# Kernel tuning notes

Hardware: AMD Instinct MI355X
Metric: run time of the kernel (lower is better)

The kernel has to match this reference:

```python
import jax, jax.numpy as jnp
import numpy as np

V = 100000  # num graph nodes
E = 800000  # num edges (avg degree 8)
B = 16      # batch
C = 16      # in == hidden == out channels (forced by residual adds)
K = 4       # Chebyshev order
EPS = 1e-5


def setup_inputs() -> dict:
    key = jax.random.key(0)
    ks = jax.random.split(key, 8)
    x = jax.random.normal(ks[0], (B, C, V), jnp.float32)
    edge_src = jax.random.randint(ks[1], (E,), 0, V, dtype=jnp.int32)
    edge_dst = jax.random.randint(ks[2], (E,), 0, V, dtype=jnp.int32)
    # small positive weights keep the Chebyshev recursion numerically tame
    edge_w = jax.random.uniform(ks[3], (E,), jnp.float32) * 0.1
    weights = jax.random.normal(ks[4], (6, K, C, C), jnp.float32) * (1.0 / np.sqrt(K * C))
    biases = jax.random.normal(ks[5], (6, C), jnp.float32) * 0.01
    gamma = jnp.ones((5, C), jnp.float32)
    beta = jnp.zeros((5, C), jnp.float32)
    return {"x": x, "edge_w": edge_w, "weights": weights, "biases": biases,
            "gamma": gamma, "beta": beta, "edge_src": edge_src, "edge_dst": edge_dst}


def reference(x, edge_w, weights, biases, gamma, beta, edge_src, edge_dst):
    def lap(xf):  # normalized laplacian apply: (2/lmax)*L - I with lmax=2 -> L - I; xf: (V, F)
        msg = xf[edge_src] * edge_w[:, None]
        return jax.ops.segment_sum(msg, edge_dst, num_segments=V) - xf

    def cheb(xin, w, b):  # xin: (B, Cin, V), w: (K, Cin, Cout), b: (Cout,)
        Cin = xin.shape[1]
        xf = xin.transpose(2, 0, 1).reshape(V, B * Cin)  # (V, B*Cin)
        x0 = xf
        xs = [x0]
        x1 = lap(x0)
        xs.append(x1)
        for _ in range(K - 2):
            x2 = 2.0 * lap(x1) - x0
            xs.append(x2)
            x0, x1 = x1, x2
        xk = jnp.stack(xs).reshape(K, V, B, Cin)
        out = jnp.einsum('kvbi,kio->bov', xk, w) + b[None, :, None]
        return out  # (B, Cout, V)

    def bn(xin, g, bt):  # BatchNorm1d over (B, C, V): stats over (B, V)
        mean = xin.mean(axis=(0, 2), keepdims=True)
        var = xin.var(axis=(0, 2), keepdims=True)
        return (xin - mean) * jax.lax.rsqrt(var + EPS) * g[None, :, None] + bt[None, :, None]

    def resblock(xin, i, bni):
        h = jax.nn.relu(cheb(xin, weights[2 * i], biases[2 * i]))
        h = bn(h, gamma[bni], beta[bni])
        h = cheb(h, weights[2 * i + 1], biases[2 * i + 1])
        return jax.nn.relu(h + xin)

    out = resblock(x, 0, 0)
    out = bn(out, gamma[3], beta[3])
    out = resblock(out, 1, 1)
    out = bn(out, gamma[4], beta[4])
    out = resblock(out, 2, 2)
    pooled = out.max(axis=2)  # MaxPool1d(num_nodes) + squeeze -> (B, C)
    return jax.nn.softmax(pooled, axis=1)
```

## Files before the change

kernel.cpp:

```cpp
#include <hip/hip_runtime.h>
#include <hip/hip_fp16.h>
#include <cstdint>

#define CAP 32
#define WAVES 4

typedef __half half_t;

__device__ __forceinline__ float4 ldh4(const half_t* p) {
  uint2 u = *reinterpret_cast<const uint2*>(p);
  __half2 h0 = *reinterpret_cast<const __half2*>(&u.x);
  __half2 h1 = *reinterpret_cast<const __half2*>(&u.y);
  float2 f0 = __half22float2(h0);
  float2 f1 = __half22float2(h1);
  return make_float4(f0.x, f0.y, f1.x, f1.y);
}

__device__ __forceinline__ void sth4(half_t* p, float x, float y, float z, float w) {
  __half2 h0 = __floats2half2_rn(x, y);
  __half2 h1 = __floats2half2_rn(z, w);
  uint2 u;
  u.x = *reinterpret_cast<unsigned int*>(&h0);
  u.y = *reinterpret_cast<unsigned int*>(&h1);
  *reinterpret_cast<uint2*>(p) = u;
}

__global__ __launch_bounds__(256) void transpose_kernel(
    const float* __restrict__ in, half_t* __restrict__ out, int V) {
  __shared__ float t[32][33];
  const int f0 = blockIdx.y * 32;
  const int v0 = blockIdx.x * 32;
  const int tid = threadIdx.x;
  const int fi = tid >> 5;
  const int vi = tid & 31;
#pragma unroll
  for (int k = 0; k < 4; ++k) {
    int f = fi + 8 * k;
    t[f][vi] = in[(size_t)(f0 + f) * V + (v0 + vi)];
  }
  __syncthreads();
  const int vl = tid >> 5;
  const int fl = tid & 31;
#pragma unroll
  for (int k = 0; k < 4; ++k) {
    int v = vl + 8 * k;
    out[(size_t)(v0 + v) * 256 + (f0 + fl)] = __float2half_rn(t[fl][v]);
  }
}

__global__ __launch_bounds__(256) void fill_kernel(
    const int* __restrict__ src, const int* __restrict__ dst,
    const float* __restrict__ w, int* __restrict__ cursor,
    int2* __restrict__ slots, int E) {
  int e = blockIdx.x * 256 + threadIdx.x;
  if (e >= E) return;
  int d = dst[e];
  int pos = atomicAdd(&cursor[d], 1);
  if (pos < CAP) slots[(size_t)d * CAP + pos] = make_int2(src[e], __float_as_int(w[e]));
}

template <int PASS, int EPI>
__global__ __launch_bounds__(256) void cheb_pass(
    const half_t* __restrict__ G, const half_t* __restrict__ Pv,
    half_t* __restrict__ D, half_t* __restrict__ O,
    const half_t* __restrict__ resid,
    const int2* __restrict__ slots, const int* __restrict__ cnt,
    const float* __restrict__ Wl, const float* __restrict__ bl,
    float* __restrict__ statsBuf, int V) {
  __shared__ float xl[WAVES][272];
  __shared__ float wl[512];
  const int tid = threadIdx.x;
  if (PASS == 1) {
    wl[tid] = Wl[tid];
    wl[256 + tid] = Wl[256 + tid];
  } else if (PASS == 2) {
    wl[tid] = Wl[512 + tid];
  } else {
    wl[tid] = Wl[768 + tid];
  }
  __syncthreads();
  const int wave = tid >> 6, lane = tid & 63;
  const int v = blockIdx.x * WAVES + wave;
  if (v >= V) return;
  const int f0 = lane << 2;
  int n = cnt[v];
  n = n > CAP ? CAP : n;
  const int2* __restrict__ row = slots + (size_t)v * CAP;
  float4 acc = make_float4(0.f, 0.f, 0.f, 0.f);
  int e = 0;
  for (; e + 2 <= n; e += 2) {
    int2 s0 = row[e];
    int2 s1 = row[e + 1];
    float w0 = __int_as_float(s0.y), w1 = __int_as_float(s1.y);
    float4 a = ldh4(G + (((size_t)s0.x) << 8) + f0);
    float4 b2 = ldh4(G + (((size_t)s1.x) << 8) + f0);
    acc.x = fmaf(w0, a.x, acc.x); acc.y = fmaf(w0, a.y, acc.y);
    acc.z = fmaf(w0, a.z, acc.z); acc.w = fmaf(w0, a.w, acc.w);
    acc.x = fmaf(w1, b2.x, acc.x); acc.y = fmaf(w1, b2.y, acc.y);
    acc.z = fmaf(w1, b2.z, acc.z); acc.w = fmaf(w1, b2.w, acc.w);
  }
  if (e < n) {
    int2 s0 = row[e];
    float w0 = __int_as_float(s0.y);
    float4 a = ldh4(G + (((size_t)s0.x) << 8) + f0);
    acc.x = fmaf(w0, a.x, acc.x); acc.y = fmaf(w0, a.y, acc.y);
    acc.z = fmaf(w0, a.z, acc.z); acc.w = fmaf(w0, a.w, acc.w);
  }
  const size_t rowoff = (((size_t)v) << 8) + f0;
  float4 g = ldh4(G + rowoff);
  float4 xn;
  if (PASS == 1) {
    xn.x = acc.x - g.x; xn.y = acc.y - g.y; xn.z = acc.z - g.z; xn.w = acc.w - g.w;
  } else {
    float4 p = ldh4(Pv + rowoff);
    xn.x = 2.f * (acc.x - g.x) - p.x;
    xn.y = 2.f * (acc.y - g.y) - p.y;
    xn.z = 2.f * (acc.z - g.z) - p.z;
    xn.w = 2.f * (acc.w - g.w) - p.w;
  }
  if (PASS != 3) {
    sth4(D + rowoff, xn.x, xn.y, xn.z, xn.w);
  }
  const int b = lane >> 2;
  const int oc = (lane & 3) << 2;
  float* xw = xl[wave];
  const int sbase = f0 + b;
  float o[4];
  if (PASS == 1) {
    o[0] = bl[oc + 0]; o[1] = bl[oc + 1]; o[2] = bl[oc + 2]; o[3] = bl[oc + 3];
    xw[sbase + 0] = g.x; xw[sbase + 1] = g.y; xw[sbase + 2] = g.z; xw[sbase + 3] = g.w;
    __builtin_amdgcn_wave_barrier();
    const float* xb = xw + b * 17;
#pragma unroll
    for (int i = 0; i < 16; ++i) {
      float xi = xb[i];
      o[0] = fmaf(xi, wl[i * 16 + oc + 0], o[0]);
      o[1] = fmaf(xi, wl[i * 16 + oc + 1], o[1]);
      o[2] = fmaf(xi, wl[i * 16 + oc + 2], o[2]);
      o[3] = fmaf(xi, wl[i * 16 + oc + 3], o[3]);
    }
    __builtin_amdgcn_wave_barrier();
  } else {
    o[0] = o[1] = o[2] = o[3] = 0.f;
  }
  xw[sbase + 0] = xn.x; xw[sbase + 1] = xn.y; xw[sbase + 2] = xn.z; xw[sbase + 3] = xn.w;
  __builtin_amdgcn_wave_barrier();
  {
    const float* xb = xw + b * 17;
    const float* wm = (PASS == 1) ? (wl + 256) : wl;
#pragma unroll
    for (int i = 0; i < 16; ++i) {
      float xi = xb[i];
      o[0] = fmaf(xi, wm[i * 16 + oc + 0], o[0]);
      o[1] = fmaf(xi, wm[i * 16 + oc + 1], o[1]);
      o[2] = fmaf(xi, wm[i * 16 + oc + 2], o[2]);
      o[3] = fmaf(xi, wm[i * 16 + oc + 3], o[3]);
    }
  }
  half_t* op = O + rowoff;
  if (PASS == 1) {
    sth4(op, o[0], o[1], o[2], o[3]);
  } else if (PASS == 2) {
    float4 c4 = ldh4(op);
    sth4(op, o[0] + c4.x, o[1] + c4.y, o[2] + c4.z, o[3] + c4.w);
  } else {
    float4 c4 = ldh4(op);
    o[0] += c4.x; o[1] += c4.y; o[2] += c4.z; o[3] += c4.w;
    if (EPI >= 2) {
      float4 r = ldh4(resid + rowoff);
      o[0] += r.x; o[1] += r.y; o[2] += r.z; o[3] += r.w;
    }
    o[0] = fmaxf(o[0], 0.f); o[1] = fmaxf(o[1], 0.f);
    o[2] = fmaxf(o[2], 0.f); o[3] = fmaxf(o[3], 0.f);
    sth4(op, o[0], o[1], o[2], o[3]);
    if (EPI == 1 || EPI == 2) {
      float s0 = o[0], s1 = o[1], s2 = o[2], s3 = o[3];
      float q0 = o[0] * o[0], q1 = o[1] * o[1], q2 = o[2] * o[2], q3 = o[3] * o[3];
#pragma unroll
      for (int d = 4; d < 64; d <<= 1) {
        s0 += __shfl_xor(s0, d); s1 += __shfl_xor(s1, d);
        s2 += __shfl_xor(s2, d); s3 += __shfl_xor(s3, d);
        q0 += __shfl_xor(q0, d); q1 += __shfl_xor(q1, d);
        q2 += __shfl_xor(q2, d); q3 += __shfl_xor(q3, d);
      }
      if (lane < 4) {
        float* sb = statsBuf + ((blockIdx.x & 63) << 5);
        atomicAdd(&sb[(lane << 2) + 0], s0);
        atomicAdd(&sb[(lane << 2) + 1], s1);
        atomicAdd(&sb[(lane << 2) + 2], s2);
        atomicAdd(&sb[(lane << 2) + 3], s3);
        atomicAdd(&sb[16 + (lane << 2) + 0], q0);
        atomicAdd(&sb[16 + (lane << 2) + 1], q1);
        atomicAdd(&sb[16 + (lane << 2) + 2], q2);
        atomicAdd(&sb[16 + (lane << 2) + 3], q3);
      }
    }
  }
}

__global__ void bn_finalize(const float* __restrict__ sb,
                            const float* __restrict__ gamma,
                            const float* __restrict__ beta,
                            float* __restrict__ affine, float invN) {
  int c = threadIdx.x;
  if (c >= 16) return;
  float s = 0.f, q = 0.f;
  for (int k = 0; k < 64; ++k) { s += sb[k * 32 + c]; q += sb[k * 32 + 16 + c]; }
  float mean = s * invN;
  float var = q * invN - mean * mean;
  float inv = rsqrtf(var + 1e-5f);
  float A = gamma[c] * inv;
  float B = beta[c] - mean * A;
  affine[c] = A;
  affine[16 + c] = B;
}

__global__ __launch_bounds__(256) void bn_apply(half_t* __restrict__ X,
                                                const float* __restrict__ affine,
                                                size_t NT) {
  size_t i0 = ((size_t)blockIdx.x * 256 + threadIdx.x) * 8;
  size_t stride = (size_t)gridDim.x * 256 * 8;
  float a[8], bb[8];
#pragma unroll
  for (int j = 0; j < 8; ++j) {
    int c = (int)((i0 + j) & 15);
    a[j] = affine[c];
    bb[j] = affine[16 + c];
  }
  for (size_t i = i0; i < NT; i += stride) {
    uint4 u = *reinterpret_cast<uint4*>(X + i);
    __half2* h = reinterpret_cast<__half2*>(&u);
#pragma unroll
    for (int j = 0; j < 4; ++j) {
      float2 f = __half22float2(h[j]);
      f.x = fmaf(a[2 * j], f.x, bb[2 * j]);
      f.y = fmaf(a[2 * j + 1], f.y, bb[2 * j + 1]);
      h[j] = __floats2half2_rn(f.x, f.y);
    }
    *reinterpret_cast<uint4*>(X + i) = u;
  }
}

__global__ __launch_bounds__(256) void pool_kernel(const half_t* __restrict__ X,
                                                   float* __restrict__ part, int V) {
  int t = threadIdx.x;
  float m = -3.402823466e38f;
  for (int v = blockIdx.x; v < V; v += gridDim.x) {
    m = fmaxf(m, __half2float(X[(((size_t)v) << 8) + t]));
  }
  part[blockIdx.x * 256 + t] = m;
}

__global__ __launch_bounds__(256) void pool_finish(const float* __restrict__ part,
                                                   float* __restrict__ out) {
  int t = threadIdx.x;
  float m = -3.402823466e38f;
  for (int k = 0; k < 256; ++k) m = fmaxf(m, part[k * 256 + t]);
  __shared__ float pm[256];
  __shared__ float mx[16], sm[16];
  pm[t] = m;
  __syncthreads();
  if (t < 16) {
    float M = -3.402823466e38f;
    for (int c = 0; c < 16; ++c) M = fmaxf(M, pm[t * 16 + c]);
    float S = 0.f;
    for (int c = 0; c < 16; ++c) S += expf(pm[t * 16 + c] - M);
    mx[t] = M;
    sm[t] = S;
  }
  __syncthreads();
  out[t] = expf(pm[t] - mx[t >> 4]) / sm[t >> 4];
}

__global__ void sentinel_kernel(float* out, float val) {
  out[threadIdx.x] = val;
}

extern "C" void kernel_launch(void* const* d_in, const int* in_sizes, int n_in,
                              void* d_out, int out_size, void* d_ws, size_t ws_size,
                              hipStream_t stream) {
  const float* x       = (const float*)d_in[0];
  const float* edge_w  = (const float*)d_in[1];
  const float* weights = (const float*)d_in[2];
  const float* biases  = (const float*)d_in[3];
  const float* gamma   = (const float*)d_in[4];
  const float* beta    = (const float*)d_in[5];
  const int*   esrc    = (const int*)d_in[6];
  const int*   edst    = (const int*)d_in[7];

  const int V = in_sizes[0] / 256;
  const int E = in_sizes[1];
  const size_t NT = (size_t)V * 256;

  char* wsp = (char*)d_ws;
  auto carve = [&](size_t bytes) {
    char* p = wsp;
    wsp += (bytes + 255) & ~(size_t)255;
    return p;
  };
  half_t* P[4];
  for (int i = 0; i < 4; ++i) P[i] = (half_t*)carve(NT * sizeof(half_t));
  int2*  slots  = (int2*)carve((size_t)V * CAP * sizeof(int2));
  int*   cursor = (int*)carve((size_t)V * sizeof(int));
  float* stats  = (float*)carve(5 * 64 * 32 * sizeof(float));
  float* affine = (float*)carve(5 * 32 * sizeof(float));
  float* part   = (float*)carve(256 * 256 * sizeof(float));
  size_t needed = (size_t)(wsp - (char*)d_ws);
  if (needed > ws_size) {
    sentinel_kernel<<<1, 256, 0, stream>>>((float*)d_out, 100.0f + (float)(needed >> 20));
    return;
  }

  hipMemsetAsync(cursor, 0, (size_t)V * sizeof(int), stream);
  hipMemsetAsync(stats, 0, 5 * 64 * 32 * sizeof(float), stream);

  dim3 tg(V / 32, 8, 1);
  transpose_kernel<<<tg, 256, 0, stream>>>(x, P[0], V);
  fill_kernel<<<(E + 255) / 256, 256, 0, stream>>>(esrc, edst, edge_w, cursor, slots, E);

  const int nb = (V + WAVES - 1) / WAVES;
  const float invN = 1.f / (16.f * (float)V);

  half_t *C = P[0], *X = P[1], *Y = P[2], *Z = P[3];
  for (int blk = 0; blk < 3; ++blk) {
    const float* WA = weights + (size_t)(2 * blk) * 1024;
    const float* WB = weights + (size_t)(2 * blk + 1) * 1024;
    const float* bA = biases + (2 * blk) * 16;
    const float* bB = biases + (2 * blk + 1) * 16;
    float* stA = stats + blk * 2048;
    float* afA = affine + blk * 32;
    cheb_pass<1, 0><<<nb, 256, 0, stream>>>(C, nullptr, X, Y, nullptr, slots, cursor, WA, bA, nullptr, V);
    cheb_pass<2, 0><<<nb, 256, 0, stream>>>(X, C, Z, Y, nullptr, slots, cursor, WA, nullptr, nullptr, V);
    cheb_pass<3, 1><<<nb, 256, 0, stream>>>(Z, X, nullptr, Y, nullptr, slots, cursor, WA, nullptr, stA, V);
    bn_finalize<<<1, 16, 0, stream>>>(stA, gamma + blk * 16, beta + blk * 16, afA, invN);
    bn_apply<<<2048, 256, 0, stream>>>(Y, afA, NT);
    cheb_pass<1, 0><<<nb, 256, 0, stream>>>(Y, nullptr, X, Z, nullptr, slots, cursor, WB, bB, nullptr, V);
    cheb_pass<2, 0><<<nb, 256, 0, stream>>>(X, Y, Y, Z, nullptr, slots, cursor, WB, nullptr, nullptr, V);
    if (blk < 2) {
      float* stI = stats + (3 + blk) * 2048;
      float* afI = affine + (3 + blk) * 32;
      cheb_pass<3, 2><<<nb, 256, 0, stream>>>(Y, X, nullptr, Z, C, slots, cursor, WB, nullptr, stI, V);
      bn_finalize<<<1, 16, 0, stream>>>(stI, gamma + (3 + blk) * 16, beta + (3 + blk) * 16, afI, invN);
      bn_apply<<<2048, 256, 0, stream>>>(Z, afI, NT);
    } else {
      cheb_pass<3, 3><<<nb, 256, 0, stream>>>(Y, X, nullptr, Z, C, slots, cursor, WB, nullptr, nullptr, V);
    }
    half_t* oC = C; half_t* oY = Y; half_t* oZ = Z;
    C = oZ; Y = oC; Z = oY;
  }
  pool_kernel<<<256, 256, 0, stream>>>(C, part, V);
  pool_finish<<<1, 256, 0, stream>>>(part, (float*)d_out);
}
```

Before: 2.374 ms.

## Batch edge slot loads via wave shuffles and unroll gathers by eight

Each wave now loads its node's 32 slot entries once, one per lane, and broadcasts source index and weight with shuffles. The neighbor loop is padded to a multiple of 8, with dummy slots pre-initialised to a self-index and zero weight, so eight independent gathers can be in flight at once. The self and previous-term loads are hoisted to the top of the kernel. This trades a new init kernel that writes all V*CAP slots, plus wasted padded gathers, for more memory-level parallelism in the sparse gather.

```diff
diff --git a/kernel.cpp b/kernel.cpp
--- a/kernel.cpp
+++ b/kernel.cpp
@@ -46,6 +46,11 @@
     int v = vl + 8 * k;
     out[(size_t)(v0 + v) * 256 + (f0 + fl)] = __float2half_rn(t[fl][v]);
   }
+}
+
+__global__ __launch_bounds__(256) void init_slots(int2* __restrict__ slots, int total) {
+  int i = blockIdx.x * 256 + threadIdx.x;
+  if (i < total) slots[i] = make_int2(i >> 5, 0);
 }
 
 __global__ __launch_bounds__(256) void fill_kernel(
@@ -83,36 +88,43 @@
   const int v = blockIdx.x * WAVES + wave;
   if (v >= V) return;
   const int f0 = lane << 2;
+  const size_t rowoff = (((size_t)v) << 8) + f0;
+
+  int2 myslot = slots[((size_t)v << 5) + (lane & 31)];
+  float4 g = ldh4(G + rowoff);
+  float4 p = make_float4(0.f, 0.f, 0.f, 0.f);
+  if (PASS != 1) p = ldh4(Pv + rowoff);
+
   int n = cnt[v];
   n = n > CAP ? CAP : n;
-  const int2* __restrict__ row = slots + (size_t)v * CAP;
+  int n8 = (n + 7) & ~7;
+
   float4 acc = make_float4(0.f, 0.f, 0.f, 0.f);
-  int e = 0;
-  for (; e + 2 <= n; e += 2) {
-    int2 s0 = row[e];
-    int2 s1 = row[e + 1];
-    float w0 = __int_as_float(s0.y), w1 = __int_as_float(s1.y);
-    float4 a = ldh4(G + (((size_t)s0.x) << 8) + f0);
-    float4 b2 = ldh4(G + (((size_t)s1.x) << 8) + f0);
-    acc.x = fmaf(w0, a.x, acc.x); acc.y = fmaf(w0, a.y, acc.y);
-    acc.z = fmaf(w0, a.z, acc.z); acc.w = fmaf(w0, a.w, acc.w);
-    acc.x = fmaf(w1, b2.x, acc.x); acc.y = fmaf(w1, b2.y, acc.y);
-    acc.z = fmaf(w1, b2.z, acc.z); acc.w = fmaf(w1, b2.w, acc.w);
-  }
-  if (e < n) {
-    int2 s0 = row[e];
-    float w0 = __int_as_float(s0.y);
-    float4 a = ldh4(G + (((size_t)s0.x) << 8) + f0);
-    acc.x = fmaf(w0, a.x, acc.x); acc.y = fmaf(w0, a.y, acc.y);
-    acc.z = fmaf(w0, a.z, acc.z); acc.w = fmaf(w0, a.w, acc.w);
-  }
-  const size_t rowoff = (((size_t)v) << 8) + f0;
-  float4 g = ldh4(G + rowoff);
+  for (int base = 0; base < n8; base += 8) {
+    const half_t* ap[8];
+    float w[8];
+#pragma unroll
+    for (int j = 0; j < 8; ++j) {
+      int s = __shfl(myslot.x, base + j);
+      w[j] = __int_as_float(__shfl(myslot.y, base + j));
+      ap[j] = G + (((size_t)s) << 8) + f0;
+    }
+    float4 a[8];
+#pragma unroll
+    for (int j = 0; j < 8; ++j) a[j] = ldh4(ap[j]);
+#pragma unroll
+    for (int j = 0; j < 8; ++j) {
+      acc.x = fmaf(w[j], a[j].x, acc.x);
+      acc.y = fmaf(w[j], a[j].y, acc.y);
+      acc.z = fmaf(w[j], a[j].z, acc.z);
+      acc.w = fmaf(w[j], a[j].w, acc.w);
+    }
+  }
+
   float4 xn;
   if (PASS == 1) {
     xn.x = acc.x - g.x; xn.y = acc.y - g.y; xn.z = acc.z - g.z; xn.w = acc.w - g.w;
   } else {
-    float4 p = ldh4(Pv + rowoff);
     xn.x = 2.f * (acc.x - g.x) - p.x;
     xn.y = 2.f * (acc.y - g.y) - p.y;
     xn.z = 2.f * (acc.z - g.z) - p.z;
@@ -313,6 +325,9 @@
 
   hipMemsetAsync(cursor, 0, (size_t)V * sizeof(int), stream);
   hipMemsetAsync(stats, 0, 5 * 64 * 32 * sizeof(float), stream);
+
+  const int totalSlots = V * CAP;
+  init_slots<<<(totalSlots + 255) / 256, 256, 0, stream>>>(slots, totalSlots);
 
   dim3 tg(V / 32, 8, 1);
   transpose_kernel<<<tg, 256, 0, stream>>>(x, P[0], V);
```

Result: faster. 2.279 ms (-4.0%).
